# Kernel optimization log

Hardware: AMD Instinct MI355X
Metric: run time of the kernel (lower is better)

The kernel has to match this reference:

```python
import jax, jax.numpy as jnp
import numpy as np
from jax import lax

B, C, P, H = 4, 3, 160, 32          # batch of box patches, channels, patch size, score-net hidden
TEMB = 64                            # time-embedding dim
BETA0, BETA1 = 0.1, 20.0             # subVP SDE beta_min / beta_max
T_EPS = 1e-5                         # integration start time (timesteps=(1e-5, 1))
N_STEPS = 10                         # (1 - eps) / ode_step_size with step_size=0.1


def _conv(x, w, b):
    y = lax.conv_general_dilated(x, w, (1, 1), 'SAME',
                                 dimension_numbers=('NCHW', 'OIHW', 'NCHW'))
    return y + b[None, :, None, None]


def _time_emb(t):
    half = TEMB // 2
    freqs = jnp.exp(-np.log(10000.0) / (half - 1) * jnp.arange(half, dtype=jnp.float32))
    a = t[:, None] * 999.0 * freqs[None, :]   # continuous t scaled as in score_sde
    return jnp.concatenate([jnp.sin(a), jnp.cos(a)], axis=-1)


def _score_net(x, t, params):
    w1, b1, wt, bt, w2, b2, w3, b3 = params
    emb = _time_emb(t) @ wt + bt                       # [B, H]
    h = jax.nn.relu(_conv(x, w1, b1) + emb[:, :, None, None])
    h = jax.nn.relu(_conv(h, w2, b2))
    return _conv(h, w3, b3)


def _drift(x, tvec, params):
    # subVP probability-flow ODE drift: f(x,t) - 0.5 * g(t)^2 * score(x,t)
    bd = BETA1 - BETA0
    beta_t = BETA0 + tvec * bd
    lmc = -0.25 * tvec ** 2 * bd - 0.5 * tvec * BETA0   # log mean coeff
    std = 1.0 - jnp.exp(2.0 * lmc)                      # marginal std
    g2 = beta_t * (1.0 - jnp.exp(4.0 * lmc))            # diffusion^2
    score = _score_net(x, tvec, params) / std[:, None, None, None]
    return -0.5 * beta_t[:, None, None, None] * x - 0.5 * g2[:, None, None, None] * score


def _forward(patches, hs_epsilon, params):
    eps = jnp.broadcast_to(hs_epsilon, patches.shape)   # fixed Rademacher probe
    dt = (1.0 - T_EPS) / N_STEPS

    def rhs(x, t):
        tvec = jnp.ones((x.shape[0],), x.dtype) * t
        # Skilling-Hutchinson divergence: eps^T J eps via one jvp
        drift, jv = jax.jvp(lambda xx: _drift(xx, tvec, params), (x,), (eps,))
        return drift, jnp.sum(jv * eps, axis=(1, 2, 3))

    def step(carry, t0):
        x, lp = carry
        k1x, k1l = rhs(x, t0)
        k2x, k2l = rhs(x + 0.5 * dt * k1x, t0 + 0.5 * dt)
        k3x, k3l = rhs(x + 0.5 * dt * k2x, t0 + 0.5 * dt)
        k4x, k4l = rhs(x + dt * k3x, t0 + dt)
        x = x + (dt / 6.0) * (k1x + 2.0 * k2x + 2.0 * k3x + k4x)
        lp = lp + (dt / 6.0) * (k1l + 2.0 * k2l + 2.0 * k3l + k4l)
        return (x, lp), None

    ts = T_EPS + dt * jnp.arange(N_STEPS, dtype=patches.dtype)
    init = (patches, jnp.zeros((patches.shape[0],), patches.dtype))
    (z, delta_logp), _ = lax.scan(jax.checkpoint(step), init, ts)

    Ndim = float(np.prod(patches.shape[1:]))
    prior_logp = -0.5 * Ndim * np.log(2.0 * np.pi) - 0.5 * jnp.sum(z ** 2, axis=(1, 2, 3))
    bpd = -(prior_logp + delta_logp) / np.log(2.0)
    return bpd / Ndim                                   # per-patch NLL (bits/dim)


def setup_inputs() -> dict:
    key = jax.random.key(0)
    ks = jax.random.split(key, 6)
    s = 0.05
    return {
        'patches': jax.random.normal(ks[0], (B, C, P, P), jnp.float32),
        'hs_epsilon': jnp.sign(jax.random.normal(ks[1], (1, C, P, P), jnp.float32)),
        'w1': jax.random.normal(ks[2], (H, C, 3, 3), jnp.float32) * s,
        'b1': jnp.zeros((H,), jnp.float32),
        'wt': jax.random.normal(ks[3], (TEMB, H), jnp.float32) * s,
        'bt': jnp.zeros((H,), jnp.float32),
        'w2': jax.random.normal(ks[4], (H, H, 3, 3), jnp.float32) * s,
        'b2': jnp.zeros((H,), jnp.float32),
        'w3': jax.random.normal(ks[5], (C, H, 3, 3), jnp.float32) * s,
        'b3': jnp.zeros((C,), jnp.float32),
    }


def reference(patches, hs_epsilon, w1, b1, wt, bt, w2, b2, w3, b3):
    params = (w1, b1, wt, bt, w2, b2, w3, b3)
    return _forward(patches, hs_epsilon, params)
```

## Files before the change

kernel.cpp:

```cpp
#include <hip/hip_runtime.h>
#include <hip/hip_bf16.h>
#include <math.h>

#define PW 160
#define PSQ 25600
#define NB 4
#define NX 307200
#define NDIM 76800

#define TY 10
#define TX 20
#define XW 26
#define XSZ 416
#define H1W 24
#define H2W 22
#define H2N 264
#define OUTN 200

typedef __attribute__((ext_vector_type(8))) short short8;
typedef __attribute__((ext_vector_type(4))) float float4v;

struct TS40 { float t[40]; };
struct MC40 { float m[40]; float A; };

__device__ __forceinline__ short bf16s(float f) {
    return __builtin_bit_cast(short, __float2bfloat16(f));
}
__device__ __forceinline__ unsigned packbf(float a, float b) {
    return (unsigned)(unsigned short)bf16s(a) | ((unsigned)(unsigned short)bf16s(b) << 16);
}

__global__ void prep_kernel(const float* __restrict__ w1, const float* __restrict__ w2,
                            const float* __restrict__ w3, short* __restrict__ w1p,
                            short* __restrict__ w2p, short* __restrict__ w3p,
                            const float* __restrict__ wt, const float* __restrict__ bt,
                            float* __restrict__ emb, TS40 ts) {
    __shared__ float e64[64];
    int blk = blockIdx.x;
    if (blk < 36) {
        int tid = blk * 256 + threadIdx.x;
        if (tid < 9216) {
            int j = tid & 7, co = (tid >> 3) & 31, q4 = tid >> 8;
            int tap = q4 >> 2, quad = q4 & 3;
            int ci = ((j >> 2) << 4) + quad * 4 + (j & 3);
            w2p[tid] = bf16s(w2[(co * 32 + ci) * 9 + tap]);
        }
        if (tid < 4608) {
            int j = tid & 7, co = (tid >> 3) & 15, q4 = tid >> 7;
            int tap = q4 >> 2, quad = q4 & 3;
            int ci = ((j >> 2) << 4) + quad * 4 + (j & 3);
            float v = (co < 3) ? w3[(co * 32 + ci) * 9 + tap] : 0.0f;
            w3p[tid] = bf16s(v);
        }
        if (tid < 1024) {
            int j = tid & 7, co = (tid >> 3) & 31, quad = tid >> 8;
            int k = quad * 8 + j;
            float v = 0.0f;
            if (k < 27) { int tap = (k * 11) >> 5; int ci = k - tap * 3; v = w1[(co * 3 + ci) * 9 + tap]; }
            w1p[tid] = bf16s(v);
        }
    } else {
        int r = blk - 36, k = threadIdx.x;
        if (k < 64) {
            float t = ts.t[r];
            int j = k & 31;
            float freq = expf(-0.29710775393471556f * (float)j);
            float a = t * 999.0f * freq;
            e64[k] = (k < 32) ? sinf(a) : cosf(a);
        }
        __syncthreads();
        if (k < 32) {
            float acc = bt[k];
            #pragma unroll 8
            for (int q = 0; q < 64; q++) acc += e64[q] * wt[q * 32 + k];
            emb[r * 32 + k] = acc;
        }
    }
}

__global__ __launch_bounds__(256) void teps_conv1(
    const float* __restrict__ xin, const short* __restrict__ w1p,
    short* __restrict__ outH) {
    const int tile = blockIdx.x;
    const int ty0 = (tile / 10) * 16, tx0 = (tile % 10) * 16;
    const int tid = threadIdx.x;
    const int lane = tid & 63, wv = tid >> 6;
    const int n = lane & 15, quad = lane >> 4;
    __shared__ float sX[3 * 324];
    for (int idx = tid; idx < 3 * 324; idx += 256) {
        int ci = idx / 324, p = idx - ci * 324;
        int ly = p / 18, lx = p - ly * 18;
        int gy = ty0 + ly - 1, gx = tx0 + lx - 1;
        float v = 0.0f;
        if (gy >= 0 && gy < PW && gx >= 0 && gx < PW)
            v = xin[(size_t)ci * PSQ + gy * PW + gx];
        sX[idx] = v;
    }
    __syncthreads();
    int offj[8], valj[8];
    #pragma unroll
    for (int j = 0; j < 8; ++j) {
        int k = quad * 8 + j;
        valj[j] = (k < 27);
        int tap = (k * 11) >> 5; if (k >= 27) tap = 0;
        int ci = k - tap * 3;
        int dy = (tap * 11) >> 5, dx = tap - dy * 3;
        offj[j] = valj[j] ? (ci * 324 + dy * 18 + dx + n) : 0;
    }
    short8 a0 = *(const short8*)&w1p[(quad * 32 + n) * 8];
    short8 a1 = *(const short8*)&w1p[(quad * 32 + 16 + n) * 8];
    #pragma unroll
    for (int r = 0; r < 4; ++r) {
        int row = wv * 4 + r;
        short8 bb;
        #pragma unroll
        for (int j = 0; j < 8; ++j) {
            float v = valj[j] ? sX[offj[j] + row * 18] : 0.0f;
            bb[j] = bf16s(v);
        }
        float4v acc0 = {0.f, 0.f, 0.f, 0.f}, acc1 = {0.f, 0.f, 0.f, 0.f};
        acc0 = __builtin_amdgcn_mfma_f32_16x16x32_bf16(a0, bb, acc0, 0, 0, 0);
        acc1 = __builtin_amdgcn_mfma_f32_16x16x32_bf16(a1, bb, acc1, 0, 0, 0);
        int pix = (ty0 + row) * PW + tx0 + n;
        uint2 h0, h1v;
        h0.x = packbf(acc0[0], acc0[1]); h0.y = packbf(acc0[2], acc0[3]);
        h1v.x = packbf(acc1[0], acc1[1]); h1v.y = packbf(acc1[2], acc1[3]);
        *(uint2*)&outH[(size_t)pix * 32 + quad * 4] = h0;
        *(uint2*)&outH[(size_t)pix * 32 + 16 + quad * 4] = h1v;
    }
}

__global__ __launch_bounds__(512, 4) void fused_stage(
    const float* __restrict__ xin, const float* __restrict__ x0r,
    float* __restrict__ x0w, float* __restrict__ xacc, float* __restrict__ xst,
    const short* __restrict__ w1p, const short* __restrict__ w2p,
    const short* __restrict__ w3p, const float* __restrict__ b1,
    const float* __restrict__ b2, const float* __restrict__ b3,
    const float* __restrict__ embr, const short* __restrict__ tepsb,
    const float* __restrict__ epsin, float* __restrict__ Sacc,
    float c1, float c2, float dt, int mode) {
    const int bid = blockIdx.x;
    const int tile = ((bid & 7) << 4) | (bid >> 3);
    const int b = blockIdx.y;
    const int oy = (tile >> 3) * TY, ox = (tile & 7) * TX;
    const int tid = threadIdx.x;
    const int lane = tid & 63, wv = tid >> 6;
    const int n = lane & 15, quad = lane >> 4;

    __shared__ __align__(16) char smem[77104];
    short* sH1 = (short*)smem;
    short* sD1 = (short*)(smem + 21504);
    short* sH2 = (short*)(smem + 43008);
    short* sD2 = (short*)(smem + 59904);
    short* sX  = (short*)(smem + 43008);
    float* sBE = (float*)(smem + 76800);
    float* sB2 = (float*)(smem + 76928);
    float* sB3 = (float*)(smem + 77056);
    float* wsum = (float*)(smem + 77072);

    uint2 pt0[3], pt1[3];
    #pragma unroll
    for (int it = 0; it < 3; ++it) {
        int t = wv + it * 8;
        int tt = (t < 21) ? t : 0;
        int p = tt * 16 + n;
        int ry = p / H1W, rx = p - ry * H1W;
        int gy = oy - 2 + ry, gx = ox - 2 + rx;
        int ok = (t < 21) && gy >= 0 && gy < PW && gx >= 0 && gx < PW;
        size_t tbase = ok ? ((size_t)(gy * PW + gx) * 32) : 0;
        pt0[it] = *(const uint2*)&tepsb[tbase + quad * 4];
        pt1[it] = *(const uint2*)&tepsb[tbase + 16 + quad * 4];
    }

    if (tid < 32) { sBE[tid] = b1[tid] + embr[tid]; sB2[tid] = b2[tid]; }
    if (tid < 3) sB3[tid] = b3[tid];

    for (int idx = tid; idx < 3 * XSZ; idx += 512) {
        int ci = idx / XSZ, p = idx - ci * XSZ;
        int ly = p / XW, lx = p - ly * XW;
        int gy = oy - 3 + ly, gx = ox - 3 + lx;
        float v = 0.0f;
        if (gy >= 0 && gy < PW && gx >= 0 && gx < PW)
            v = xin[(size_t)(b * 3 + ci) * PSQ + gy * PW + gx];
        sX[idx] = bf16s(v);
    }
    __syncthreads();

    {
        int koff[8], kval[8];
        #pragma unroll
        for (int j = 0; j < 8; ++j) {
            int k = quad * 8 + j;
            kval[j] = (k < 27);
            int tap = (k * 11) >> 5; if (k >= 27) tap = 0;
            int ci = k - tap * 3;
            int dy = (tap * 11) >> 5, dx = tap - dy * 3;
            koff[j] = kval[j] ? (ci * XSZ + dy * XW + dx) : 0;
        }
        short8 a0 = *(const short8*)&w1p[(quad * 32 + n) * 8];
        short8 a1 = *(const short8*)&w1p[(quad * 32 + 16 + n) * 8];
        #pragma unroll
        for (int it = 0; it < 3; ++it) {
            int t = wv + it * 8;
            if (t < 21) {
                int p = t * 16 + n;
                int ry = p / H1W, rx = p - ry * H1W;
                int gy = oy - 2 + ry, gx = ox - 2 + rx;
                int inimg = (gy >= 0 && gy < PW && gx >= 0 && gx < PW);
                int base = ry * XW + rx;
                short8 bb;
                #pragma unroll
                for (int j = 0; j < 8; ++j)
                    bb[j] = kval[j] ? sX[koff[j] + base] : (short)0;
                float4v acc0 = {0.f, 0.f, 0.f, 0.f}, acc1 = {0.f, 0.f, 0.f, 0.f};
                acc0 = __builtin_amdgcn_mfma_f32_16x16x32_bf16(a0, bb, acc0, 0, 0, 0);
                acc1 = __builtin_amdgcn_mfma_f32_16x16x32_bf16(a1, bb, acc1, 0, 0, 0);
                int swz = (p & 7) << 4;
                unsigned hq[4], dq[4];
                #pragma unroll
                for (int mt = 0; mt < 2; ++mt) {
                    float4v* ac = mt ? &acc1 : &acc0;
                    uint2 t2 = mt ? pt1[it] : pt0[it];
                    int co0 = mt * 16 + quad * 4;
                    unsigned ts4[4] = {t2.x & 0xFFFFu, t2.x >> 16, t2.y & 0xFFFFu, t2.y >> 16};
                    unsigned hv[4], dv[4];
                    #pragma unroll
                    for (int g = 0; g < 4; ++g) {
                        float pre = (*ac)[g] + sBE[co0 + g];
                        hv[g] = inimg ? (unsigned)(unsigned short)bf16s(fmaxf(pre, 0.0f)) : 0u;
                        dv[g] = (inimg && pre > 0.0f) ? ts4[g] : 0u;
                    }
                    hq[mt * 2]     = hv[0] | (hv[1] << 16);
                    hq[mt * 2 + 1] = hv[2] | (hv[3] << 16);
                    dq[mt * 2]     = dv[0] | (dv[1] << 16);
                    dq[mt * 2 + 1] = dv[2] | (dv[3] << 16);
                }
                int byw = ((p << 6) | (quad << 4)) ^ swz;
                uint4 H4 = {hq[0], hq[1], hq[2], hq[3]};
                uint4 D4 = {dq[0], dq[1], dq[2], dq[3]};
                *(uint4*)((char*)sH1 + byw) = H4;
                *(uint4*)((char*)sD1 + byw) = D4;
            }
        }
    }
    __syncthreads();

    {
        short8 a2[9][2];
        #pragma unroll
        for (int tap = 0; tap < 9; ++tap) {
            a2[tap][0] = *(const short8*)&w2p[((tap * 4 + quad) * 32 + n) * 8];
            a2[tap][1] = *(const short8*)&w2p[((tap * 4 + quad) * 32 + 16 + n) * 8];
        }
        for (int t = wv; t < 17; t += 8) {
            int p = t * 16 + n;
            int pc = p < H2N ? p : (H2N - 1);
            int ry = pc / H2W, rx = pc - ry * H2W;
            float4v aP0 = {0.f,0.f,0.f,0.f}, aP1 = {0.f,0.f,0.f,0.f};
            float4v aD0 = {0.f,0.f,0.f,0.f}, aD1 = {0.f,0.f,0.f,0.f};
            #pragma unroll
            for (int tap = 0; tap < 9; ++tap) {
                int dy = (tap * 11) >> 5, dx = tap - dy * 3;
                int q = (ry + dy) * H1W + rx + dx;
                int byr = ((q << 6) | (quad << 4)) ^ ((q & 7) << 4);
                short8 bp = *(const short8*)((const char*)sH1 + byr);
                short8 bd = *(const short8*)((const char*)sD1 + byr);
                aP0 = __builtin_amdgcn_mfma_f32_16x16x32_bf16(a2[tap][0], bp, aP0, 0, 0, 0);
                aP1 = __builtin_amdgcn_mfma_f32_16x16x32_bf16(a2[tap][1], bp, aP1, 0, 0, 0);
                aD0 = __builtin_amdgcn_mfma_f32_16x16x32_bf16(a2[tap][0], bd, aD0, 0, 0, 0);
                aD1 = __builtin_amdgcn_mfma_f32_16x16x32_bf16(a2[tap][1], bd, aD1, 0, 0, 0);
            }
            int gy = oy - 1 + ry, gx = ox - 1 + rx;
            int inimg = (gy >= 0 && gy < PW && gx >= 0 && gx < PW);
            if (p < H2N) {
                int swz = (p & 7) << 4;
                unsigned hq[4], dq[4];
                #pragma unroll
                for (int mt = 0; mt < 2; ++mt) {
                    float4v* acP = mt ? &aP1 : &aP0;
                    float4v* acD = mt ? &aD1 : &aD0;
                    int co0 = mt * 16 + quad * 4;
                    unsigned hv[4], dv[4];
                    #pragma unroll
                    for (int g = 0; g < 4; ++g) {
                        float pre = (*acP)[g] + sB2[co0 + g];
                        hv[g] = inimg ? (unsigned)(unsigned short)bf16s(fmaxf(pre, 0.0f)) : 0u;
                        dv[g] = (inimg && pre > 0.0f) ? (unsigned)(unsigned short)bf16s((*acD)[g]) : 0u;
                    }
                    hq[mt * 2]     = hv[0] | (hv[1] << 16);
                    hq[mt * 2 + 1] = hv[2] | (hv[3] << 16);
                    dq[mt * 2]     = dv[0] | (dv[1] << 16);
                    dq[mt * 2 + 1] = dv[2] | (dv[3] << 16);
                }
                int byw = ((p << 6) | (quad << 4)) ^ swz;
                uint4 H4 = {hq[0], hq[1], hq[2], hq[3]};
                uint4 D4 = {dq[0], dq[1], dq[2], dq[3]};
                *(uint4*)((char*)sH2 + byw) = H4;
                *(uint4*)((char*)sD2 + byw) = D4;
            }
        }
    }
    __syncthreads();

    float s = 0.0f;
    {
        short8 a3[9];
        #pragma unroll
        for (int tap = 0; tap < 9; ++tap)
            a3[tap] = *(const short8*)&w3p[((tap * 4 + quad) * 16 + n) * 8];
        for (int t = wv; t < 13; t += 8) {
            int p = t * 16 + n;
            int pc = p < OUTN ? p : (OUTN - 1);
            int ry = pc / TX, rx = pc - ry * TX;
            int act = (quad == 0 && p < OUTN);
            int pix = (oy + ry) * PW + ox + rx;
            float fx[3], fe[3], fa[3], f0[3];
            #pragma unroll
            for (int c = 0; c < 3; ++c) {
                size_t gi = (size_t)(b * 3 + c) * PSQ + pix;
                fx[c] = act ? xin[gi] : 0.0f;
                fe[c] = act ? epsin[c * PSQ + pix] : 0.0f;
                fa[c] = 0.0f; f0[c] = 0.0f;
                if (mode >= 1) {
                    fa[c] = act ? xacc[gi] : 0.0f;
                    f0[c] = act ? x0r[gi] : 0.0f;
                }
            }
            float4v aP = {0.f,0.f,0.f,0.f}, aD = {0.f,0.f,0.f,0.f};
            #pragma unroll
            for (int tap = 0; tap < 9; ++tap) {
                int dy = (tap * 11) >> 5, dx = tap - dy * 3;
                int q = (ry + dy) * H2W + rx + dx;
                int byr = ((q << 6) | (quad << 4)) ^ ((q & 7) << 4);
                short8 bp = *(const short8*)((const char*)sH2 + byr);
                short8 bd = *(const short8*)((const char*)sD2 + byr);
                aP = __builtin_amdgcn_mfma_f32_16x16x32_bf16(a3[tap], bp, aP, 0, 0, 0);
                aD = __builtin_amdgcn_mfma_f32_16x16x32_bf16(a3[tap], bd, aD, 0, 0, 0);
            }
            if (act) {
                #pragma unroll
                for (int c = 0; c < 3; ++c) {
                    float y = aP[c] + sB3[c];
                    float d = aD[c];
                    float xv = fx[c];
                    float k = -c1 * xv - c2 * y;
                    size_t gi = (size_t)(b * 3 + c) * PSQ + pix;
                    if (mode == 0) {
                        xacc[gi] = k;
                        xst[gi] = xv + 0.5f * dt * k;
                    } else if (mode == 1) {
                        xacc[gi] = fa[c] + 2.0f * k;
                        xst[gi] = f0[c] + 0.5f * dt * k;
                    } else if (mode == 2) {
                        xacc[gi] = fa[c] + 2.0f * k;
                        xst[gi] = f0[c] + dt * k;
                    } else {
                        x0w[gi] = f0[c] + (dt / 6.0f) * (fa[c] + k);
                    }
                    s += d * fe[c];
                }
            }
        }
    }
    #pragma unroll
    for (int off = 32; off > 0; off >>= 1) s += __shfl_down(s, off);
    if (lane == 0) wsum[wv] = s;
    __syncthreads();
    if (tid == 0) {
        float tot = 0.0f;
        #pragma unroll
        for (int w = 0; w < 8; ++w) tot += wsum[w];
        atomicAdd(&Sacc[b], tot);
    }
}

__global__ void sumz2_kernel(const float* __restrict__ x0, float* __restrict__ sumz2) {
    int b = blockIdx.x, seg = blockIdx.y, tid = threadIdx.x;
    const float* p = x0 + (size_t)b * NDIM + seg * 3072;
    float s = 0.0f;
    for (int i = tid; i < 3072; i += 256) { float v = p[i]; s += v * v; }
    #pragma unroll
    for (int off = 32; off > 0; off >>= 1) s += __shfl_down(s, off);
    __shared__ float wsum[4];
    if ((tid & 63) == 0) wsum[tid >> 6] = s;
    __syncthreads();
    if (tid == 0) atomicAdd(&sumz2[b], wsum[0] + wsum[1] + wsum[2] + wsum[3]);
}

__global__ void bpd_kernel(const float* __restrict__ S, const float* __restrict__ sumz2,
                           float* __restrict__ out, MC40 mc) {
    int b = threadIdx.x;
    if (b >= NB) return;
    float lp = mc.A;
    for (int r = 0; r < 40; r++) lp -= mc.m[r] * S[r * 4 + b];
    float prior = -70574.479354f - 0.5f * sumz2[b];
    out[b] = -(prior + lp) * 1.8785164100960743e-5f;
}

extern "C" void kernel_launch(void* const* d_in, const int* in_sizes, int n_in,
                              void* d_out, int out_size, void* d_ws, size_t ws_size,
                              hipStream_t stream) {
    const float* patches = (const float*)d_in[0];
    const float* epsin = (const float*)d_in[1];
    const float* w1 = (const float*)d_in[2];
    const float* b1 = (const float*)d_in[3];
    const float* wt = (const float*)d_in[4];
    const float* bt = (const float*)d_in[5];
    const float* w2 = (const float*)d_in[6];
    const float* b2 = (const float*)d_in[7];
    const float* w3 = (const float*)d_in[8];
    const float* b3 = (const float*)d_in[9];
    float* outp = (float*)d_out;
    char* wsb = (char*)d_ws;

    float* Sbuf  = (float*)(wsb + 0);
    float* sumz2 = (float*)(wsb + 640);
    float* emb   = (float*)(wsb + 1024);
    short* w1p   = (short*)(wsb + 6144);
    short* w2p   = (short*)(wsb + 8192);
    short* w3p   = (short*)(wsb + 26624);
    short* tepsb = (short*)(wsb + 36864);
    float* x0ws  = (float*)(wsb + 1675264);
    float* xacc  = (float*)(wsb + 2904064);
    float* xst   = (float*)(wsb + 4132864);

    const double dt = (1.0 - 1e-5) / 10.0;
    TS40 ts; MC40 mc;
    float c1a[40], c2a[40];
    double A = 0.0;
    const double wgt[4] = {1.0, 2.0, 2.0, 1.0};
    for (int i = 0; i < 10; i++) {
        double t0 = 1e-5 + dt * i;
        double tr[4] = {t0, t0 + 0.5 * dt, t0 + 0.5 * dt, t0 + dt};
        for (int s = 0; s < 4; s++) {
            int r = i * 4 + s;
            double t = tr[s];
            double beta = 0.1 + 19.9 * t;
            double lmc = -0.25 * t * t * 19.9 - 0.05 * t;
            double stdv = 1.0 - exp(2.0 * lmc);
            double g2 = beta * (1.0 - exp(4.0 * lmc));
            double c2 = 0.5 * g2 / stdv;
            ts.t[r] = (float)t;
            c1a[r] = (float)(0.5 * beta);
            c2a[r] = (float)c2;
            double coef = dt / 6.0 * wgt[s];
            mc.m[r] = (float)(coef * c2);
            A += coef * (-0.5 * beta * (double)NDIM);
        }
    }
    mc.A = (float)A;

    hipMemsetAsync(wsb, 0, 656, stream);

    prep_kernel<<<76, 256, 0, stream>>>(w1, w2, w3, w1p, w2p, w3p, wt, bt, emb, ts);
    teps_conv1<<<100, 256, 0, stream>>>(epsin, w1p, tepsb);

    for (int i = 0; i < 10; i++) {
        const float* x0r = (i == 0) ? patches : x0ws;
        for (int s = 0; s < 4; s++) {
            int r = i * 4 + s;
            const float* xin = (s == 0) ? x0r : xst;
            fused_stage<<<dim3(128, NB), 512, 0, stream>>>(
                xin, x0r, x0ws, xacc, xst, w1p, w2p, w3p, b1, b2, b3,
                emb + r * 32, tepsb, epsin, Sbuf + r * 4,
                c1a[r], c2a[r], (float)dt, s);
        }
    }
    sumz2_kernel<<<dim3(NB, 25), 256, 0, stream>>>(x0ws, sumz2);
    bpd_kernel<<<1, 64, 0, stream>>>(Sbuf, sumz2, outp, mc);
}
```

Baseline: 851.6 us.

## Read conv1 input from a padded bf16 global mirror instead of LDS staging

Each stage now also writes its output state as bf16 into a zero-padded global mirror buffer. The next stage's first convolution gathers its inputs directly from that mirror instead of loading, bounds-checking and converting the float input into shared memory. This removes the staging loop and its conversions and shrinks LDS use, at the cost of extra global writes and scattered per-element global reads in the conv1 gather. The per-block reduction through shared memory is also replaced with one atomic per wave, which drops a barrier but adds more atomics.

```diff
diff --git a/kernel.cpp b/kernel.cpp
--- a/kernel.cpp
+++ b/kernel.cpp
@@ -10,13 +10,14 @@
 
 #define TY 10
 #define TX 20
-#define XW 26
-#define XSZ 416
 #define H1W 24
 #define H2W 22
 #define H2N 264
 #define OUTN 200
 
+#define MIRW 166
+#define MIRS 27556
+
 typedef __attribute__((ext_vector_type(8))) short short8;
 typedef __attribute__((ext_vector_type(4))) float float4v;
 
@@ -34,7 +35,8 @@
                             const float* __restrict__ w3, short* __restrict__ w1p,
                             short* __restrict__ w2p, short* __restrict__ w3p,
                             const float* __restrict__ wt, const float* __restrict__ bt,
-                            float* __restrict__ emb, TS40 ts) {
+                            float* __restrict__ emb, const float* __restrict__ patches,
+                            short* __restrict__ patH, TS40 ts) {
     __shared__ float e64[64];
     int blk = blockIdx.x;
     if (blk < 36) {
@@ -59,7 +61,7 @@
             if (k < 27) { int tap = (k * 11) >> 5; int ci = k - tap * 3; v = w1[(co * 3 + ci) * 9 + tap]; }
             w1p[tid] = bf16s(v);
         }
-    } else {
+    } else if (blk < 76) {
         int r = blk - 36, k = threadIdx.x;
         if (k < 64) {
             float t = ts.t[r];
@@ -74,6 +76,14 @@
             #pragma unroll 8
             for (int q = 0; q < 64; q++) acc += e64[q] * wt[q * 32 + k];
             emb[r * 32 + k] = acc;
+        }
+    } else {
+        int idx = (blk - 76) * 256 + threadIdx.x;
+        if (idx < NX) {
+            int bc = idx / PSQ;
+            int rem = idx - bc * PSQ;
+            int py = rem / PW, px = rem - py * PW;
+            patH[(size_t)bc * MIRS + (py + 3) * MIRW + (px + 3)] = bf16s(patches[idx]);
         }
     }
 }
@@ -133,6 +143,7 @@
 __global__ __launch_bounds__(512, 4) void fused_stage(
     const float* __restrict__ xin, const float* __restrict__ x0r,
     float* __restrict__ x0w, float* __restrict__ xacc, float* __restrict__ xst,
+    const short* __restrict__ xinH, short* __restrict__ mirw,
     const short* __restrict__ w1p, const short* __restrict__ w2p,
     const short* __restrict__ w3p, const float* __restrict__ b1,
     const float* __restrict__ b2, const float* __restrict__ b3,
@@ -147,16 +158,14 @@
     const int lane = tid & 63, wv = tid >> 6;
     const int n = lane & 15, quad = lane >> 4;
 
-    __shared__ __align__(16) char smem[77104];
+    __shared__ __align__(16) char smem[77056];
     short* sH1 = (short*)smem;
     short* sD1 = (short*)(smem + 21504);
     short* sH2 = (short*)(smem + 43008);
     short* sD2 = (short*)(smem + 59904);
-    short* sX  = (short*)(smem + 43008);
     float* sBE = (float*)(smem + 76800);
     float* sB2 = (float*)(smem + 76928);
-    float* sB3 = (float*)(smem + 77056);
-    float* wsum = (float*)(smem + 77072);
+    float* sB3 = (float*)(smem + 76992);
 
     uint2 pt0[3], pt1[3];
     #pragma unroll
@@ -174,19 +183,10 @@
 
     if (tid < 32) { sBE[tid] = b1[tid] + embr[tid]; sB2[tid] = b2[tid]; }
     if (tid < 3) sB3[tid] = b3[tid];
-
-    for (int idx = tid; idx < 3 * XSZ; idx += 512) {
-        int ci = idx / XSZ, p = idx - ci * XSZ;
-        int ly = p / XW, lx = p - ly * XW;
-        int gy = oy - 3 + ly, gx = ox - 3 + lx;
-        float v = 0.0f;
-        if (gy >= 0 && gy < PW && gx >= 0 && gx < PW)
-            v = xin[(size_t)(b * 3 + ci) * PSQ + gy * PW + gx];
-        sX[idx] = bf16s(v);
-    }
     __syncthreads();
 
     {
+        const short* xb = xinH + (size_t)b * 3 * MIRS;
         int koff[8], kval[8];
         #pragma unroll
         for (int j = 0; j < 8; ++j) {
@@ -195,7 +195,7 @@
             int tap = (k * 11) >> 5; if (k >= 27) tap = 0;
             int ci = k - tap * 3;
             int dy = (tap * 11) >> 5, dx = tap - dy * 3;
-            koff[j] = kval[j] ? (ci * XSZ + dy * XW + dx) : 0;
+            koff[j] = kval[j] ? (ci * MIRS + dy * MIRW + dx) : 0;
         }
         short8 a0 = *(const short8*)&w1p[(quad * 32 + n) * 8];
         short8 a1 = *(const short8*)&w1p[(quad * 32 + 16 + n) * 8];
@@ -207,11 +207,11 @@
                 int ry = p / H1W, rx = p - ry * H1W;
                 int gy = oy - 2 + ry, gx = ox - 2 + rx;
                 int inimg = (gy >= 0 && gy < PW && gx >= 0 && gx < PW);
-                int base = ry * XW + rx;
+                int base = (oy + ry) * MIRW + (ox + rx);
                 short8 bb;
                 #pragma unroll
                 for (int j = 0; j < 8; ++j)
-                    bb[j] = kval[j] ? sX[koff[j] + base] : (short)0;
+                    bb[j] = kval[j] ? xb[koff[j] + base] : (short)0;
                 float4v acc0 = {0.f, 0.f, 0.f, 0.f}, acc1 = {0.f, 0.f, 0.f, 0.f};
                 acc0 = __builtin_amdgcn_mfma_f32_16x16x32_bf16(a0, bb, acc0, 0, 0, 0);
                 acc1 = __builtin_amdgcn_mfma_f32_16x16x32_bf16(a1, bb, acc1, 0, 0, 0);
@@ -338,6 +338,7 @@
                 aD = __builtin_amdgcn_mfma_f32_16x16x32_bf16(a3[tap], bd, aD, 0, 0, 0);
             }
             if (act) {
+                size_t mbase = (size_t)b * 3 * MIRS + (oy + ry + 3) * MIRW + (ox + rx + 3);
                 #pragma unroll
                 for (int c = 0; c < 3; ++c) {
                     float y = aP[c] + sB3[c];
@@ -345,18 +346,24 @@
                     float xv = fx[c];
                     float k = -c1 * xv - c2 * y;
                     size_t gi = (size_t)(b * 3 + c) * PSQ + pix;
+                    float outv;
                     if (mode == 0) {
                         xacc[gi] = k;
-                        xst[gi] = xv + 0.5f * dt * k;
+                        outv = xv + 0.5f * dt * k;
+                        xst[gi] = outv;
                     } else if (mode == 1) {
                         xacc[gi] = fa[c] + 2.0f * k;
-                        xst[gi] = f0[c] + 0.5f * dt * k;
+                        outv = f0[c] + 0.5f * dt * k;
+                        xst[gi] = outv;
                     } else if (mode == 2) {
                         xacc[gi] = fa[c] + 2.0f * k;
-                        xst[gi] = f0[c] + dt * k;
+                        outv = f0[c] + dt * k;
+                        xst[gi] = outv;
                     } else {
-                        x0w[gi] = f0[c] + (dt / 6.0f) * (fa[c] + k);
+                        outv = f0[c] + (dt / 6.0f) * (fa[c] + k);
+                        x0w[gi] = outv;
                     }
+                    mirw[mbase + (size_t)c * MIRS] = bf16s(outv);
                     s += d * fe[c];
                 }
             }
@@ -364,14 +371,7 @@
     }
     #pragma unroll
     for (int off = 32; off > 0; off >>= 1) s += __shfl_down(s, off);
-    if (lane == 0) wsum[wv] = s;
-    __syncthreads();
-    if (tid == 0) {
-        float tot = 0.0f;
-        #pragma unroll
-        for (int w = 0; w < 8; ++w) tot += wsum[w];
-        atomicAdd(&Sacc[b], tot);
-    }
+    if (lane == 0) atomicAdd(&Sacc[b], s);
 }
 
 __global__ void sumz2_kernel(const float* __restrict__ x0, float* __restrict__ sumz2) {
@@ -423,6 +423,9 @@
     float* x0ws  = (float*)(wsb + 1675264);
     float* xacc  = (float*)(wsb + 2904064);
     float* xst   = (float*)(wsb + 4132864);
+    short* patH  = (short*)(wsb + 5361664);
+    short* x0H   = (short*)(wsb + 6023008);
+    short* xstH  = (short*)(wsb + 6684352);
 
     const double dt = (1.0 - 1e-5) / 10.0;
     TS40 ts; MC40 mc;
@@ -451,17 +454,23 @@
     mc.A = (float)A;
 
     hipMemsetAsync(wsb, 0, 656, stream);
-
-    prep_kernel<<<76, 256, 0, stream>>>(w1, w2, w3, w1p, w2p, w3p, wt, bt, emb, ts);
+    hipMemsetAsync(wsb + 5361664, 0, 3 * 661344, stream);
+
+    prep_kernel<<<1276, 256, 0, stream>>>(w1, w2, w3, w1p, w2p, w3p,
+                                          wt, bt, emb, patches, patH, ts);
     teps_conv1<<<100, 256, 0, stream>>>(epsin, w1p, tepsb);
 
     for (int i = 0; i < 10; i++) {
         const float* x0r = (i == 0) ? patches : x0ws;
+        const short* x0rH = (i == 0) ? patH : x0H;
         for (int s = 0; s < 4; s++) {
             int r = i * 4 + s;
             const float* xin = (s == 0) ? x0r : xst;
+            const short* xinH = (s == 0) ? x0rH : xstH;
+            short* mirw = (s < 3) ? xstH : x0H;
             fused_stage<<<dim3(128, NB), 512, 0, stream>>>(
-                xin, x0r, x0ws, xacc, xst, w1p, w2p, w3p, b1, b2, b3,
+                xin, x0r, x0ws, xacc, xst, xinH, mirw,
+                w1p, w2p, w3p, b1, b2, b3,
                 emb + r * 32, tepsb, epsin, Sbuf + r * 4,
                 c1a[r], c2a[r], (float)dt, s);
         }
```

New measurement: 2.644 ms. +210.5%, slower.
